# Optimization experiments

Hardware: AMD Instinct MI355X
Metric: run time of the kernel (lower is better)

The kernel has to match this reference:

```python
import jax, jax.numpy as jnp
import numpy as np

CH = 128
GROUPS = 8
EPS = 1e-5


def setup_inputs() -> dict:
    key = jax.random.key(0)
    ks = jax.random.split(key, 12)
    b, c, h, w = 16, CH, 64, 64
    x = jax.random.normal(ks[0], (b, c, h, w), dtype=jnp.float32)
    s = 1.0 / np.sqrt(c)
    return {
        "x": x,
        "gn_w": jnp.ones((c,), jnp.float32),
        "gn_b": jnp.zeros((c,), jnp.float32),
        "wq": jax.random.normal(ks[1], (c, c), jnp.float32) * s,
        "bq": jax.random.normal(ks[2], (c,), jnp.float32) * 0.01,
        "wk": jax.random.normal(ks[3], (c, c), jnp.float32) * s,
        "bk": jax.random.normal(ks[4], (c,), jnp.float32) * 0.01,
        "wv": jax.random.normal(ks[5], (c, c), jnp.float32) * s,
        "bv": jax.random.normal(ks[6], (c,), jnp.float32) * 0.01,
        "wf": jax.random.normal(ks[7], (c, c), jnp.float32) * s,
        "bf": jax.random.normal(ks[8], (c,), jnp.float32) * 0.01,
    }


def _group_norm(x, gamma, beta):
    b, c, h, w = x.shape
    xg = x.reshape(b, GROUPS, -1)  # [b, g, (c/g)*h*w]
    mean = xg.mean(axis=-1, keepdims=True)
    var = xg.var(axis=-1, keepdims=True)
    xn = ((xg - mean) * jax.lax.rsqrt(var + EPS)).reshape(b, c, h, w)
    return xn * gamma[None, :, None, None] + beta[None, :, None, None]


def reference(x, gn_w, gn_b, wq, bq, wk, bk, wv, bv, wf, bf):
    b, c, h, w = x.shape
    x_gn = _group_norm(x, gn_w, gn_b)
    xf = x_gn.reshape(b, c, h * w)  # [b, c, n]
    # 1x1 convs == per-position channel matmuls
    q = jnp.einsum('oc,bcn->bon', wq, xf) + bq[None, :, None]
    k = jnp.einsum('oc,bcn->bon', wk, xf) + bk[None, :, None]
    v = jnp.einsum('oc,bcn->bon', wv, xf) + bv[None, :, None]
    scale = c ** (-0.5)
    attn = jnp.einsum('bci,bcj->bij', q, k) * scale  # [b, n, n]
    attn = jax.nn.softmax(attn, axis=-1)
    # out[b,c,i] = sum_j v[b,c,j] * attn[b,i,j]
    o = jnp.einsum('bcj,bij->bci', v, attn)
    of = jnp.einsum('oc,bcn->bon', wf, o) + bf[None, :, None]
    return of.reshape(b, c, h, w) + x
```

## Files before the change

### kernel.cpp

```cpp
#include <hip/hip_runtime.h>

#define NB   16
#define NC   128
#define NPOS 4096

typedef short bf16x8 __attribute__((ext_vector_type(8)));
typedef float f32x4  __attribute__((ext_vector_type(4)));
typedef float f32x16 __attribute__((ext_vector_type(16)));
typedef unsigned int u32x4 __attribute__((ext_vector_type(4)));

#define SCF 0.12751743075095855f

static __device__ __forceinline__ unsigned short f2bf(float f) {
    unsigned int u = __builtin_bit_cast(unsigned int, f);
    u += 0x7FFFu + ((u >> 16) & 1u);
    return (unsigned short)(u >> 16);
}

static __device__ __forceinline__ unsigned int pkbf(float hi, float lo) {
    return __builtin_amdgcn_perm(__builtin_bit_cast(unsigned int, hi),
                                 __builtin_bit_cast(unsigned int, lo), 0x07060302u);
}

static __device__ __forceinline__ float vmax16(const f32x16 v) {
    float a = fmaxf(fmaxf(v[0], v[1]), fmaxf(v[2], v[3]));
    float b = fmaxf(fmaxf(v[4], v[5]), fmaxf(v[6], v[7]));
    float c = fmaxf(fmaxf(v[8], v[9]), fmaxf(v[10], v[11]));
    float d = fmaxf(fmaxf(v[12], v[13]), fmaxf(v[14], v[15]));
    return fmaxf(fmaxf(a, b), fmaxf(c, d));
}

static __device__ __forceinline__ float vsum16(const float* p) {
    float a = (p[0] + p[1]) + (p[2] + p[3]);
    float b = (p[4] + p[5]) + (p[6] + p[7]);
    float c = (p[8] + p[9]) + (p[10] + p[11]);
    float d = (p[12] + p[13]) + (p[14] + p[15]);
    return (a + b) + (c + d);
}

static __device__ __forceinline__ void mk_bfrag_pair(const float* pp, bf16x8* dst, int h) {
    #pragma unroll
    for (int c2 = 0; c2 < 2; ++c2) {
        int rb = c2 * 8;
        unsigned int A0 = pkbf(pp[rb + 1], pp[rb + 0]);
        unsigned int A1 = pkbf(pp[rb + 3], pp[rb + 2]);
        unsigned int B0 = pkbf(pp[rb + 5], pp[rb + 4]);
        unsigned int B1 = pkbf(pp[rb + 7], pp[rb + 6]);
        unsigned int s0 = h ? A0 : B0, s1 = h ? A1 : B1;
        unsigned int r0 = __shfl_xor(s0, 32), r1 = __shfl_xor(s1, 32);
        u32x4 f;
        f[0] = h ? r0 : A0; f[1] = h ? r1 : A1;
        f[2] = h ? B0 : r0; f[3] = h ? B1 : r1;
        dst[c2] = __builtin_bit_cast(bf16x8, f);
    }
}

__global__ void wconv_kernel(const float* __restrict__ wq, const float* __restrict__ wk,
                             const float* __restrict__ wv, const float* __restrict__ wf,
                             unsigned short* __restrict__ oq, unsigned short* __restrict__ ok,
                             unsigned short* __restrict__ ov, unsigned short* __restrict__ of) {
    int i = blockIdx.x * 256 + threadIdx.x;
    oq[i] = f2bf(wq[i]); ok[i] = f2bf(wk[i]); ov[i] = f2bf(wv[i]); of[i] = f2bf(wf[i]);
}

__global__ void gnstat_kernel(const float* __restrict__ x, float* __restrict__ mean,
                              float* __restrict__ rstd) {
    int bg = blockIdx.x;
    const float* p = x + (size_t)bg * 65536;
    int t = threadIdx.x;
    float s = 0.f, q = 0.f;
    for (int it = 0; it < 64; ++it) {
        f32x4 v = *(const f32x4*)(p + it * 1024 + t * 4);
        s += v[0] + v[1] + v[2] + v[3];
        q += v[0] * v[0] + v[1] * v[1] + v[2] * v[2] + v[3] * v[3];
    }
    for (int m = 1; m < 64; m <<= 1) { s += __shfl_xor(s, m); q += __shfl_xor(q, m); }
    __shared__ float ls[4], lq[4];
    int w = t >> 6;
    if ((t & 63) == 0) { ls[w] = s; lq[w] = q; }
    __syncthreads();
    if (t == 0) {
        s = ls[0] + ls[1] + ls[2] + ls[3];
        q = lq[0] + lq[1] + lq[2] + lq[3];
        float mu  = s * (1.0f / 65536.0f);
        float var = q * (1.0f / 65536.0f) - mu * mu;
        mean[bg] = mu;
        rstd[bg] = rsqrtf(var + 1e-5f);
    }
}

__global__ __launch_bounds__(256) void qkv_kernel(
    const float* __restrict__ x, const float* __restrict__ gnw, const float* __restrict__ gnb,
    const float* __restrict__ mean, const float* __restrict__ rstd,
    const unsigned short* __restrict__ wqb, const unsigned short* __restrict__ wkb,
    const unsigned short* __restrict__ wvb,
    const float* __restrict__ bq, const float* __restrict__ bk, const float* __restrict__ bv,
    unsigned short* __restrict__ qT, unsigned short* __restrict__ Kf, unsigned short* __restrict__ Vf) {
    __shared__ __attribute__((aligned(16))) unsigned short xn[64 * 136];
    __shared__ __attribute__((aligned(16))) unsigned short bnc[64 * 128];
    const int b = blockIdx.y, i0 = blockIdx.x * 64, jt = blockIdx.x;
    const int t = threadIdx.x;
    {
        int iL = (t & 15) * 4;
        int cb = (t >> 4) * 2;
        for (int cg = 0; cg < 4; ++cg) {
            int c = cg * 32 + cb;
            int g = c >> 4;
            float mu = mean[b * 8 + g], rs = rstd[b * 8 + g];
            float ga0 = gnw[c] * rs,     be0 = gnb[c]     - mu * ga0;
            float ga1 = gnw[c + 1] * rs, be1 = gnb[c + 1] - mu * ga1;
            const float* p0 = x + ((size_t)(b * NC + c)) * NPOS + i0 + iL;
            f32x4 v0 = *(const f32x4*)p0;
            f32x4 v1 = *(const f32x4*)(p0 + NPOS);
            for (int e = 0; e < 4; ++e) {
                unsigned int u = (unsigned)f2bf(v0[e] * ga0 + be0) |
                                 ((unsigned)f2bf(v1[e] * ga1 + be1) << 16);
                *(unsigned int*)&xn[(iL + e) * 136 + c] = u;
            }
        }
    }
    __syncthreads();

    const int lane = t & 63, w = t >> 6, quad = lane >> 4, li = lane & 15;

    bf16x8 ax[4];
    for (int kc = 0; kc < 4; ++kc)
        ax[kc] = *(const bf16x8*)&xn[(w * 16 + li) * 136 + kc * 32 + quad * 8];

    for (int wt = 0; wt < 2; ++wt) {
        const unsigned short* W = wt ? wkb : wqb;
        const float* bias = wt ? bk : bq;
        const float osc = wt ? 1.0f : SCF;
        for (int nt = 0; nt < 8; ++nt) {
            f32x4 d = {0.f, 0.f, 0.f, 0.f};
            for (int kc = 0; kc < 4; ++kc) {
                bf16x8 bw = *(const bf16x8*)&W[(nt * 16 + li) * 128 + kc * 32 + quad * 8];
                d = __builtin_amdgcn_mfma_f32_16x16x32_bf16(ax[kc], bw, d, 0, 0, 0);
            }
            float bb = bias[nt * 16 + li];
            int o = nt * 16 + li;
            for (int rr = 0; rr < 4; ++rr) {
                int i = w * 16 + quad * 4 + rr;
                bnc[i * 128 + (((o >> 3) ^ (i & 7)) << 3) + (o & 7)] = f2bf((d[rr] + bb) * osc);
            }
        }
        __syncthreads();
        if (wt == 0) {
            unsigned short* dst = qT + ((size_t)b * NPOS + i0) * NC + t * 32;
            int i = t >> 2;
            for (int s = 0; s < 4; ++s) {
                int cc = (t & 3) * 4 + s;
                *(bf16x8*)(dst + s * 8) = *(const bf16x8*)&bnc[i * 128 + ((cc ^ (i & 7)) << 3)];
            }
        } else {
            unsigned short* dst = Kf + ((size_t)(b * 64 + jt)) * 8192 + t * 32;
            int F = t >> 4, jtile = F >> 3, kc = F & 7;
            for (int s = 0; s < 4; ++s) {
                int L = (t * 4 + s) & 63;
                int i = jtile * 32 + (L & 31);
                int cc = kc * 2 + (L >> 5);
                *(bf16x8*)(dst + s * 8) = *(const bf16x8*)&bnc[i * 128 + ((cc ^ (i & 7)) << 3)];
            }
        }
        __syncthreads();
    }

    bf16x8 av[2][4];
    for (int mt = 0; mt < 2; ++mt)
        for (int kc = 0; kc < 4; ++kc)
            av[mt][kc] = *(const bf16x8*)&wvb[((w * 2 + mt) * 16 + li) * 128 + kc * 32 + quad * 8];
    for (int nt = 0; nt < 4; ++nt) {
        bf16x8 bx[4];
        for (int kc = 0; kc < 4; ++kc)
            bx[kc] = *(const bf16x8*)&xn[(nt * 16 + li) * 136 + kc * 32 + quad * 8];
        for (int mt = 0; mt < 2; ++mt) {
            f32x4 d = {0.f, 0.f, 0.f, 0.f};
            for (int kc = 0; kc < 4; ++kc)
                d = __builtin_amdgcn_mfma_f32_16x16x32_bf16(av[mt][kc], bx[kc], d, 0, 0, 0);
            int o0 = (w * 2 + mt) * 16 + quad * 4;
            int j = nt * 16 + li;
            for (int rr = 0; rr < 4; ++rr) {
                int c = o0 + rr;
                bnc[c * 64 + (((j >> 3) ^ (c & 7)) << 3) + (j & 7)] = f2bf(d[rr] + bv[c]);
            }
        }
    }
    __syncthreads();
    {
        unsigned short* dst = Vf + ((size_t)(b * 64 + jt)) * 8192 + t * 32;
        int F = t >> 4, ct = F >> 2, kc2 = F & 3;
        for (int s = 0; s < 4; ++s) {
            int L = (t * 4 + s) & 63;
            int c = ct * 32 + (L & 31);
            int jc = kc2 * 2 + (L >> 5);
            *(bf16x8*)(dst + s * 8) = *(const bf16x8*)&bnc[c * 64 + ((jc ^ (c & 7)) << 3)];
        }
    }
}

static __device__ __forceinline__ void flash_iter(
    bf16x8 (&kcur)[16], bf16x8 (&knxt)[16],
    const unsigned short*& kp, const unsigned short*& vp,
    const bf16x8 (&qb)[2][8], float (&mr)[2], float (&lr)[2],
    f32x16 (&acc)[2][4], const int h) {
    bf16x8 vf[16];
    #pragma unroll
    for (int m = 0; m < 16; ++m) vf[m] = *(const bf16x8*)(vp + m * 512);
    vp += 8192;
    #pragma unroll
    for (int m = 0; m < 16; ++m) knxt[m] = *(const bf16x8*)(kp + m * 512);
    kp += 8192;

    f32x16 st[4];
    #pragma unroll
    for (int u = 0; u < 4; ++u)
        #pragma unroll
        for (int q = 0; q < 16; ++q) st[u][q] = 0.f;
    #pragma unroll
    for (int kc = 0; kc < 8; ++kc) {
        st[0] = __builtin_amdgcn_mfma_f32_32x32x16_bf16(kcur[kc],     qb[0][kc], st[0], 0, 0, 0);
        st[1] = __builtin_amdgcn_mfma_f32_32x32x16_bf16(kcur[8 + kc], qb[0][kc], st[1], 0, 0, 0);
        st[2] = __builtin_amdgcn_mfma_f32_32x32x16_bf16(kcur[kc],     qb[1][kc], st[2], 0, 0, 0);
        st[3] = __builtin_amdgcn_mfma_f32_32x32x16_bf16(kcur[8 + kc], qb[1][kc], st[3], 0, 0, 0);
    }

    #pragma unroll
    for (int ig = 0; ig < 2; ++ig) {
        float mx = fmaxf(vmax16(st[ig * 2]), vmax16(st[ig * 2 + 1]));
        mx = fmaxf(mx, __shfl_xor(mx, 32));
        if (__any(mx > mr[ig])) {
            float mn = fmaxf(mr[ig], mx);
            float alpha = __builtin_amdgcn_exp2f(mr[ig] - mn);
            mr[ig] = mn;
            lr[ig] *= alpha;
            #pragma unroll
            for (int ct = 0; ct < 4; ++ct)
                #pragma unroll
                for (int q = 0; q < 16; ++q) acc[ig][ct][q] *= alpha;
        }
        float mc = mr[ig] - 0.0028150156f;
        float p0[16], p1[16];
        #pragma unroll
        for (int q = 0; q < 16; ++q) {
            p0[q] = __builtin_amdgcn_exp2f(st[ig * 2][q] - mc);
            p1[q] = __builtin_amdgcn_exp2f(st[ig * 2 + 1][q] - mc);
        }
        float rs = vsum16(p0) + vsum16(p1);
        rs += __shfl_xor(rs, 32);
        lr[ig] += rs;

        bf16x8 pfrag[4];
        mk_bfrag_pair(p0, &pfrag[0], h);
        mk_bfrag_pair(p1, &pfrag[2], h);

        #pragma unroll
        for (int ct = 0; ct < 4; ++ct)
            #pragma unroll
            for (int kc2 = 0; kc2 < 4; ++kc2)
                acc[ig][ct] = __builtin_amdgcn_mfma_f32_32x32x16_bf16(vf[ct * 4 + kc2], pfrag[kc2],
                                                                      acc[ig][ct], 0, 0, 0);
    }
}

__global__ __launch_bounds__(128, 1) void flash_kernel(
    const unsigned short* __restrict__ qT, const unsigned short* __restrict__ Kf,
    const unsigned short* __restrict__ Vf, const unsigned short* __restrict__ wfb,
    const float* __restrict__ bf_, const float* __restrict__ x, float* __restrict__ out) {
    const int idx = blockIdx.x;
    const int b = (idx & 7) * 2 + ((idx >> 3) & 1);
    const int r = idx >> 4;
    const int t = threadIdx.x, lane = t & 63, w = t >> 6;
    const int il = lane & 31, h = lane >> 5;
    const int iw = r * 128 + w * 64;

    bf16x8 qb[2][8];
    #pragma unroll
    for (int ig = 0; ig < 2; ++ig)
        #pragma unroll
        for (int kc = 0; kc < 8; ++kc)
            qb[ig][kc] = *(const bf16x8*)&qT[((size_t)b * NPOS + iw + ig * 32 + il) * NC + kc * 16 + h * 8];

    float mr[2] = {-1e30f, -1e30f}, lr[2] = {0.f, 0.f};
    f32x16 acc[2][4];
    #pragma unroll
    for (int ig = 0; ig < 2; ++ig)
        #pragma unroll
        for (int ct = 0; ct < 4; ++ct)
            #pragma unroll
            for (int q = 0; q < 16; ++q) acc[ig][ct][q] = 0.f;

    const unsigned short* kp = Kf + ((size_t)b * 64) * 8192 + lane * 8;
    const unsigned short* vp = Vf + ((size_t)b * 64) * 8192 + lane * 8;

    bf16x8 kA[16], kB[16];
    #pragma unroll
    for (int m = 0; m < 16; ++m) kA[m] = *(const bf16x8*)(kp + m * 512);
    kp += 8192;

    for (int jo = 0; jo < 32; ++jo) {
        flash_iter(kA, kB, kp, vp, qb, mr, lr, acc, h);
        flash_iter(kB, kA, kp, vp, qb, mr, lr, acc, h);
    }

    bf16x8 obf[2][8];
    #pragma unroll
    for (int ig = 0; ig < 2; ++ig) {
        float inv = __builtin_amdgcn_rcpf(lr[ig]) * 1.001953125f;
        #pragma unroll
        for (int ct = 0; ct < 4; ++ct) {
            float pp[16];
            #pragma unroll
            for (int q = 0; q < 16; ++q) pp[q] = acc[ig][ct][q] * inv;
            mk_bfrag_pair(pp, &obf[ig][ct * 2], h);
        }
    }

    #pragma unroll
    for (int ot = 0; ot < 4; ++ot) {
        bf16x8 wfA[8];
        #pragma unroll
        for (int kc = 0; kc < 8; ++kc)
            wfA[kc] = *(const bf16x8*)&wfb[(ot * 32 + il) * 128 + kc * 16 + h * 8];
        #pragma unroll
        for (int ig = 0; ig < 2; ++ig) {
            f32x16 d;
            #pragma unroll
            for (int q = 0; q < 16; ++q) d[q] = 0.f;
            #pragma unroll
            for (int kc = 0; kc < 8; ++kc)
                d = __builtin_amdgcn_mfma_f32_32x32x16_bf16(wfA[kc], obf[ig][kc], d, 0, 0, 0);
            const int ig_i = iw + ig * 32 + il;
            #pragma unroll
            for (int q = 0; q < 16; ++q) {
                int o = ot * 32 + (q & 3) + 8 * (q >> 2) + 4 * h;
                size_t a = ((size_t)(b * NC + o)) * NPOS + ig_i;
                out[a] = d[q] + bf_[o] + x[a];
            }
        }
    }
}

extern "C" void kernel_launch(void* const* d_in, const int* in_sizes, int n_in,
                              void* d_out, int out_size, void* d_ws, size_t ws_size,
                              hipStream_t stream) {
    const float* x   = (const float*)d_in[0];
    const float* gnw = (const float*)d_in[1];
    const float* gnb = (const float*)d_in[2];
    const float* wq  = (const float*)d_in[3];
    const float* bq  = (const float*)d_in[4];
    const float* wk  = (const float*)d_in[5];
    const float* bk  = (const float*)d_in[6];
    const float* wv  = (const float*)d_in[7];
    const float* bv  = (const float*)d_in[8];
    const float* wf  = (const float*)d_in[9];
    const float* bf_ = (const float*)d_in[10];
    float* out = (float*)d_out;

    char* ws = (char*)d_ws;
    float* mean = (float*)(ws + 0);
    float* rstd = (float*)(ws + 512);
    unsigned short* wqb = (unsigned short*)(ws + 1024);
    unsigned short* wkb = wqb + 16384;
    unsigned short* wvb = wkb + 16384;
    unsigned short* wfb = wvb + 16384;
    unsigned short* qT  = (unsigned short*)(ws + 132096);
    unsigned short* Kf  = qT + (size_t)NB * NPOS * NC;
    unsigned short* Vf  = Kf + (size_t)NB * NPOS * NC;

    wconv_kernel<<<64, 256, 0, stream>>>(wq, wk, wv, wf, wqb, wkb, wvb, wfb);
    gnstat_kernel<<<128, 256, 0, stream>>>(x, mean, rstd);
    dim3 g(64, 16);
    qkv_kernel<<<g, 256, 0, stream>>>(x, gnw, gnb, mean, rstd, wqb, wkb, wvb, bq, bk, bv, qT, Kf, Vf);
    flash_kernel<<<512, 128, 0, stream>>>(qT, Kf, Vf, wfb, bf_, x, out);
}
```

Baseline: 332.4 us.

## Split KV sequence across two waves per block and merge softmax states via LDS

Each block now covers 64 query rows instead of 128, and its two waves each process half of the key/value sequence for the same rows. The partial accumulators, running max and running sum are then merged through shared memory using flash-decoding style rescaling. The grid doubles to 1024 blocks and launch bounds allow two blocks per CU, which is meant to improve occupancy and load balance on the many-CU GPU. The cost is an LDS round-trip, two barriers and duplicated Q loads across waves, and register pressure may rise or spill under the tighter launch bound.

```diff
diff --git a/kernel.cpp b/kernel.cpp
--- a/kernel.cpp
+++ b/kernel.cpp
@@ -262,16 +262,17 @@
     }
 }
 
-__global__ __launch_bounds__(128, 1) void flash_kernel(
+__global__ __launch_bounds__(128, 2) void flash_kernel(
     const unsigned short* __restrict__ qT, const unsigned short* __restrict__ Kf,
     const unsigned short* __restrict__ Vf, const unsigned short* __restrict__ wfb,
     const float* __restrict__ bf_, const float* __restrict__ x, float* __restrict__ out) {
+    __shared__ __attribute__((aligned(16))) float smrg[8192 + 256];
     const int idx = blockIdx.x;
     const int b = (idx & 7) * 2 + ((idx >> 3) & 1);
-    const int r = idx >> 4;
+    const int rg = idx >> 4;
     const int t = threadIdx.x, lane = t & 63, w = t >> 6;
     const int il = lane & 31, h = lane >> 5;
-    const int iw = r * 128 + w * 64;
+    const int iw = rg * 64;
 
     bf16x8 qb[2][8];
     #pragma unroll
@@ -289,34 +290,78 @@
             #pragma unroll
             for (int q = 0; q < 16; ++q) acc[ig][ct][q] = 0.f;
 
-    const unsigned short* kp = Kf + ((size_t)b * 64) * 8192 + lane * 8;
-    const unsigned short* vp = Vf + ((size_t)b * 64) * 8192 + lane * 8;
+    const unsigned short* kp = Kf + ((size_t)(b * 64 + w * 32)) * 8192 + lane * 8;
+    const unsigned short* vp = Vf + ((size_t)(b * 64 + w * 32)) * 8192 + lane * 8;
 
     bf16x8 kA[16], kB[16];
     #pragma unroll
     for (int m = 0; m < 16; ++m) kA[m] = *(const bf16x8*)(kp + m * 512);
     kp += 8192;
 
-    for (int jo = 0; jo < 32; ++jo) {
+    for (int jo = 0; jo < 16; ++jo) {
         flash_iter(kA, kB, kp, vp, qb, mr, lr, acc, h);
         flash_iter(kB, kA, kp, vp, qb, mr, lr, acc, h);
     }
 
-    bf16x8 obf[2][8];
-    #pragma unroll
-    for (int ig = 0; ig < 2; ++ig) {
-        float inv = __builtin_amdgcn_rcpf(lr[ig]) * 1.001953125f;
+    const int po = 1 - w;
+    f32x4* sv = (f32x4*)smrg;
+    float* sml = smrg + 8192;
+    #pragma unroll
+    for (int ct = 0; ct < 4; ++ct)
+        #pragma unroll
+        for (int qq = 0; qq < 4; ++qq) {
+            f32x4 tv;
+            #pragma unroll
+            for (int e = 0; e < 4; ++e) tv[e] = acc[po][ct][qq * 4 + e];
+            sv[(po * 16 + ct * 4 + qq) * 64 + lane] = tv;
+        }
+    sml[po * 128 + lane] = mr[po];
+    sml[po * 128 + 64 + lane] = lr[po];
+    __syncthreads();
+    {
+        float m1 = sml[w * 128 + lane], l1 = sml[w * 128 + 64 + lane];
+        float mn = fmaxf(mr[w], m1);
+        float a0 = __builtin_amdgcn_exp2f(mr[w] - mn);
+        float a1 = __builtin_amdgcn_exp2f(m1 - mn);
+        lr[w] = lr[w] * a0 + l1 * a1;
+        #pragma unroll
+        for (int ct = 0; ct < 4; ++ct)
+            #pragma unroll
+            for (int qq = 0; qq < 4; ++qq) {
+                f32x4 tv = sv[(w * 16 + ct * 4 + qq) * 64 + lane];
+                #pragma unroll
+                for (int e = 0; e < 4; ++e)
+                    acc[w][ct][qq * 4 + e] = acc[w][ct][qq * 4 + e] * a0 + tv[e] * a1;
+            }
+    }
+    {
+        float inv = __builtin_amdgcn_rcpf(lr[w]) * 1.001953125f;
+        bf16x8* so = (bf16x8*)smrg;
         #pragma unroll
         for (int ct = 0; ct < 4; ++ct) {
             float pp[16];
             #pragma unroll
-            for (int q = 0; q < 16; ++q) pp[q] = acc[ig][ct][q] * inv;
-            mk_bfrag_pair(pp, &obf[ig][ct * 2], h);
-        }
-    }
-
-    #pragma unroll
-    for (int ot = 0; ot < 4; ++ot) {
+            for (int q = 0; q < 16; ++q) pp[q] = acc[w][ct][q] * inv;
+            bf16x8 fr[2];
+            mk_bfrag_pair(pp, fr, h);
+            so[(w * 16 + ct * 2) * 64 + lane]     = fr[0];
+            so[(w * 16 + ct * 2 + 1) * 64 + lane] = fr[1];
+        }
+    }
+    __syncthreads();
+    bf16x8 obf[2][8];
+    {
+        const bf16x8* so = (const bf16x8*)smrg;
+        #pragma unroll
+        for (int ig = 0; ig < 2; ++ig)
+            #pragma unroll
+            for (int kc = 0; kc < 8; ++kc)
+                obf[ig][kc] = so[(ig * 16 + kc) * 64 + lane];
+    }
+
+    #pragma unroll
+    for (int op = 0; op < 2; ++op) {
+        const int ot = w * 2 + op;
         bf16x8 wfA[8];
         #pragma unroll
         for (int kc = 0; kc < 8; ++kc)
@@ -371,5 +416,5 @@
     gnstat_kernel<<<128, 256, 0, stream>>>(x, mean, rstd);
     dim3 g(64, 16);
     qkv_kernel<<<g, 256, 0, stream>>>(x, gnw, gnb, mean, rstd, wqb, wkb, wvb, bq, bk, bv, qT, Kf, Vf);
-    flash_kernel<<<512, 128, 0, stream>>>(qT, Kf, Vf, wfb, bf_, x, out);
-}
+    flash_kernel<<<1024, 128, 0, stream>>>(qT, Kf, Vf, wfb, bf_, x, out);
+}
```

After: 638.3 us. +92.0%, slower.

## Shrink per-wave query tile to 32 rows, use 4 waves and 2 blocks/CU

Applied to the files above, without the earlier changes.

Each wave now handles 32 query rows instead of 64, and blocks grow to 256 threads with launch bounds allowing 2 blocks per CU. This roughly quarters accumulator and K/V register footprint, so more waves can be resident to hide global K/V load latency. The K double buffer is replaced by a single buffer reloaded after the QK MFMAs, and V is loaded per tile. In exchange each K/V fragment loaded from global/L2 is reused by half as many query rows, doubling K/V load traffic per unit of work.

```diff
diff --git a/kernel.cpp b/kernel.cpp
--- a/kernel.cpp
+++ b/kernel.cpp
@@ -198,120 +198,100 @@
     }
 }
 
-static __device__ __forceinline__ void flash_iter(
-    bf16x8 (&kcur)[16], bf16x8 (&knxt)[16],
-    const unsigned short*& kp, const unsigned short*& vp,
-    const bf16x8 (&qb)[2][8], float (&mr)[2], float (&lr)[2],
-    f32x16 (&acc)[2][4], const int h) {
-    bf16x8 vf[16];
-    #pragma unroll
-    for (int m = 0; m < 16; ++m) vf[m] = *(const bf16x8*)(vp + m * 512);
-    vp += 8192;
-    #pragma unroll
-    for (int m = 0; m < 16; ++m) knxt[m] = *(const bf16x8*)(kp + m * 512);
-    kp += 8192;
-
-    f32x16 st[4];
-    #pragma unroll
-    for (int u = 0; u < 4; ++u)
-        #pragma unroll
-        for (int q = 0; q < 16; ++q) st[u][q] = 0.f;
-    #pragma unroll
-    for (int kc = 0; kc < 8; ++kc) {
-        st[0] = __builtin_amdgcn_mfma_f32_32x32x16_bf16(kcur[kc],     qb[0][kc], st[0], 0, 0, 0);
-        st[1] = __builtin_amdgcn_mfma_f32_32x32x16_bf16(kcur[8 + kc], qb[0][kc], st[1], 0, 0, 0);
-        st[2] = __builtin_amdgcn_mfma_f32_32x32x16_bf16(kcur[kc],     qb[1][kc], st[2], 0, 0, 0);
-        st[3] = __builtin_amdgcn_mfma_f32_32x32x16_bf16(kcur[8 + kc], qb[1][kc], st[3], 0, 0, 0);
-    }
-
-    #pragma unroll
-    for (int ig = 0; ig < 2; ++ig) {
-        float mx = fmaxf(vmax16(st[ig * 2]), vmax16(st[ig * 2 + 1]));
-        mx = fmaxf(mx, __shfl_xor(mx, 32));
-        if (__any(mx > mr[ig])) {
-            float mn = fmaxf(mr[ig], mx);
-            float alpha = __builtin_amdgcn_exp2f(mr[ig] - mn);
-            mr[ig] = mn;
-            lr[ig] *= alpha;
-            #pragma unroll
-            for (int ct = 0; ct < 4; ++ct)
-                #pragma unroll
-                for (int q = 0; q < 16; ++q) acc[ig][ct][q] *= alpha;
-        }
-        float mc = mr[ig] - 0.0028150156f;
-        float p0[16], p1[16];
-        #pragma unroll
-        for (int q = 0; q < 16; ++q) {
-            p0[q] = __builtin_amdgcn_exp2f(st[ig * 2][q] - mc);
-            p1[q] = __builtin_amdgcn_exp2f(st[ig * 2 + 1][q] - mc);
-        }
-        float rs = vsum16(p0) + vsum16(p1);
-        rs += __shfl_xor(rs, 32);
-        lr[ig] += rs;
-
-        bf16x8 pfrag[4];
-        mk_bfrag_pair(p0, &pfrag[0], h);
-        mk_bfrag_pair(p1, &pfrag[2], h);
-
-        #pragma unroll
-        for (int ct = 0; ct < 4; ++ct)
-            #pragma unroll
-            for (int kc2 = 0; kc2 < 4; ++kc2)
-                acc[ig][ct] = __builtin_amdgcn_mfma_f32_32x32x16_bf16(vf[ct * 4 + kc2], pfrag[kc2],
-                                                                      acc[ig][ct], 0, 0, 0);
-    }
-}
-
-__global__ __launch_bounds__(128, 1) void flash_kernel(
+__global__ __launch_bounds__(256, 2) void flash_kernel(
     const unsigned short* __restrict__ qT, const unsigned short* __restrict__ Kf,
     const unsigned short* __restrict__ Vf, const unsigned short* __restrict__ wfb,
     const float* __restrict__ bf_, const float* __restrict__ x, float* __restrict__ out) {
     const int idx = blockIdx.x;
     const int b = (idx & 7) * 2 + ((idx >> 3) & 1);
-    const int r = idx >> 4;
+    const int rg = idx >> 4;
     const int t = threadIdx.x, lane = t & 63, w = t >> 6;
     const int il = lane & 31, h = lane >> 5;
-    const int iw = r * 128 + w * 64;
-
-    bf16x8 qb[2][8];
-    #pragma unroll
-    for (int ig = 0; ig < 2; ++ig)
-        #pragma unroll
-        for (int kc = 0; kc < 8; ++kc)
-            qb[ig][kc] = *(const bf16x8*)&qT[((size_t)b * NPOS + iw + ig * 32 + il) * NC + kc * 16 + h * 8];
-
-    float mr[2] = {-1e30f, -1e30f}, lr[2] = {0.f, 0.f};
-    f32x16 acc[2][4];
-    #pragma unroll
-    for (int ig = 0; ig < 2; ++ig)
+    const int iw = (rg * 4 + w) * 32;
+
+    bf16x8 qb[8];
+    #pragma unroll
+    for (int kc = 0; kc < 8; ++kc)
+        qb[kc] = *(const bf16x8*)&qT[((size_t)b * NPOS + iw + il) * NC + kc * 16 + h * 8];
+
+    float mr = -1e30f, lr = 0.f;
+    f32x16 acc[4];
+    #pragma unroll
+    for (int ct = 0; ct < 4; ++ct)
+        #pragma unroll
+        for (int q = 0; q < 16; ++q) acc[ct][q] = 0.f;
+
+    const unsigned short* kp = Kf + ((size_t)b * 64) * 8192 + lane * 8;
+    const unsigned short* vp = Vf + ((size_t)b * 64) * 8192 + lane * 8;
+
+    bf16x8 kf[16];
+    #pragma unroll
+    for (int m = 0; m < 16; ++m) kf[m] = *(const bf16x8*)(kp + m * 512);
+    kp += 8192;
+
+    for (int jt = 0; jt < 64; ++jt) {
+        f32x16 st[2];
+        #pragma unroll
+        for (int u = 0; u < 2; ++u)
+            #pragma unroll
+            for (int q = 0; q < 16; ++q) st[u][q] = 0.f;
+        #pragma unroll
+        for (int kc = 0; kc < 8; ++kc) {
+            st[0] = __builtin_amdgcn_mfma_f32_32x32x16_bf16(kf[kc],     qb[kc], st[0], 0, 0, 0);
+            st[1] = __builtin_amdgcn_mfma_f32_32x32x16_bf16(kf[8 + kc], qb[kc], st[1], 0, 0, 0);
+        }
+        #pragma unroll
+        for (int m = 0; m < 16; ++m) kf[m] = *(const bf16x8*)(kp + m * 512);
+        kp += 8192;
+
+        float mx = fmaxf(vmax16(st[0]), vmax16(st[1]));
+        mx = fmaxf(mx, __shfl_xor(mx, 32));
+        if (__any(mx > mr)) {
+            float mn = fmaxf(mr, mx);
+            float alpha = __builtin_amdgcn_exp2f(mr - mn);
+            mr = mn;
+            lr *= alpha;
+            #pragma unroll
+            for (int ct = 0; ct < 4; ++ct)
+                #pragma unroll
+                for (int q = 0; q < 16; ++q) acc[ct][q] *= alpha;
+        }
+        float mc = mr - 0.0028150156f;
+        #pragma unroll
+        for (int q = 0; q < 16; ++q) {
+            st[0][q] = __builtin_amdgcn_exp2f(st[0][q] - mc);
+            st[1][q] = __builtin_amdgcn_exp2f(st[1][q] - mc);
+        }
+        float rs = vsum16((const float*)&st[0]) + vsum16((const float*)&st[1]);
+        rs += __shfl_xor(rs, 32);
+        lr += rs;
+
+        bf16x8 pfrag[4];
+        mk_bfrag_pair((const float*)&st[0], &pfrag[0], h);
+        mk_bfrag_pair((const float*)&st[1], &pfrag[2], h);
+
+        bf16x8 vf[16];
+        #pragma unroll
+        for (int m = 0; m < 16; ++m) vf[m] = *(const bf16x8*)(vp + m * 512);
+        vp += 8192;
+
         #pragma unroll
         for (int ct = 0; ct < 4; ++ct)
             #pragma unroll
-            for (int q = 0; q < 16; ++q) acc[ig][ct][q] = 0.f;
-
-    const unsigned short* kp = Kf + ((size_t)b * 64) * 8192 + lane * 8;
-    const unsigned short* vp = Vf + ((size_t)b * 64) * 8192 + lane * 8;
-
-    bf16x8 kA[16], kB[16];
-    #pragma unroll
-    for (int m = 0; m < 16; ++m) kA[m] = *(const bf16x8*)(kp + m * 512);
-    kp += 8192;
-
-    for (int jo = 0; jo < 32; ++jo) {
-        flash_iter(kA, kB, kp, vp, qb, mr, lr, acc, h);
-        flash_iter(kB, kA, kp, vp, qb, mr, lr, acc, h);
-    }
-
-    bf16x8 obf[2][8];
-    #pragma unroll
-    for (int ig = 0; ig < 2; ++ig) {
-        float inv = __builtin_amdgcn_rcpf(lr[ig]) * 1.001953125f;
+            for (int kc2 = 0; kc2 < 4; ++kc2)
+                acc[ct] = __builtin_amdgcn_mfma_f32_32x32x16_bf16(vf[ct * 4 + kc2], pfrag[kc2],
+                                                                  acc[ct], 0, 0, 0);
+    }
+
+    bf16x8 obf[8];
+    {
+        float inv = __builtin_amdgcn_rcpf(lr) * 1.001953125f;
         #pragma unroll
         for (int ct = 0; ct < 4; ++ct) {
             float pp[16];
             #pragma unroll
-            for (int q = 0; q < 16; ++q) pp[q] = acc[ig][ct][q] * inv;
-            mk_bfrag_pair(pp, &obf[ig][ct * 2], h);
+            for (int q = 0; q < 16; ++q) pp[q] = acc[ct][q] * inv;
+            mk_bfrag_pair(pp, &obf[ct * 2], h);
         }
     }
 
@@ -321,21 +301,18 @@
         #pragma unroll
         for (int kc = 0; kc < 8; ++kc)
             wfA[kc] = *(const bf16x8*)&wfb[(ot * 32 + il) * 128 + kc * 16 + h * 8];
-        #pragma unroll
-        for (int ig = 0; ig < 2; ++ig) {
-            f32x16 d;
-            #pragma unroll
-            for (int q = 0; q < 16; ++q) d[q] = 0.f;
-            #pragma unroll
-            for (int kc = 0; kc < 8; ++kc)
-                d = __builtin_amdgcn_mfma_f32_32x32x16_bf16(wfA[kc], obf[ig][kc], d, 0, 0, 0);
-            const int ig_i = iw + ig * 32 + il;
-            #pragma unroll
-            for (int q = 0; q < 16; ++q) {
-                int o = ot * 32 + (q & 3) + 8 * (q >> 2) + 4 * h;
-                size_t a = ((size_t)(b * NC + o)) * NPOS + ig_i;
-                out[a] = d[q] + bf_[o] + x[a];
-            }
+        f32x16 d;
+        #pragma unroll
+        for (int q = 0; q < 16; ++q) d[q] = 0.f;
+        #pragma unroll
+        for (int kc = 0; kc < 8; ++kc)
+            d = __builtin_amdgcn_mfma_f32_32x32x16_bf16(wfA[kc], obf[kc], d, 0, 0, 0);
+        const int gi = iw + il;
+        #pragma unroll
+        for (int q = 0; q < 16; ++q) {
+            int o = ot * 32 + (q & 3) + 8 * (q >> 2) + 4 * h;
+            size_t a = ((size_t)(b * NC + o)) * NPOS + gi;
+            out[a] = d[q] + bf_[o] + x[a];
         }
     }
 }
@@ -371,5 +348,5 @@
     gnstat_kernel<<<128, 256, 0, stream>>>(x, mean, rstd);
     dim3 g(64, 16);
     qkv_kernel<<<g, 256, 0, stream>>>(x, gnw, gnb, mean, rstd, wqb, wkb, wvb, bq, bk, bv, qT, Kf, Vf);
-    flash_kernel<<<512, 128, 0, stream>>>(qT, Kf, Vf, wfb, bf_, x, out);
-}
+    flash_kernel<<<512, 256, 0, stream>>>(qT, Kf, Vf, wfb, bf_, x, out);
+}
```

Result: slower. 341.5 us (+2.8%).
